# Kernel tuning notes

Measured on AMD Instinct MI355X. Metric: run time of the kernel, lower is better.

The kernel has to match this reference:

```python
import jax, jax.numpy as jnp
import numpy as np

HIND = 512
D = 256
P = 512          # 2*d Givens rotations
RHO_MAX = 9.0
DELTA = 1e-3
EPS = 1e-8
B = 32768


def setup_inputs() -> dict:
    key = jax.random.key(0)
    ks = jax.random.split(key, 12)
    f = lambda k, shape, sc=1.0: jax.random.normal(k, shape, dtype=jnp.float32) * sc
    return {
        "ent_embed": f(ks[0], (B, HIND)),
        "rel_embed": f(ks[1], (B, HIND)),
        "ent_label": f(ks[2], (B, HIND)),
        "sim": jax.random.uniform(ks[3], (B,), dtype=jnp.float32),
        # W_v: Linear(hind, d)
        "Wv": f(ks[4], (D, HIND), 0.05), "bv": jnp.zeros((D,), jnp.float32),
        # w_rho_ent: Linear(hind, 1), bias init 0.5
        "Wre": f(ks[5], (1, HIND), 0.05), "bre": jnp.full((1,), 0.5, jnp.float32),
        # w_rho_rel: Linear(hind, 1)
        "Wrr": f(ks[6], (1, HIND), 0.05), "brr": jnp.zeros((1,), jnp.float32),
        # W_theta: Linear(hind, P)
        "Wt": f(ks[7], (P, HIND), 0.05), "bt": jnp.zeros((P,), jnp.float32),
        "ga_rho": jnp.array([2.0], jnp.float32), "gb_rho": jnp.array([-0.5], jnp.float32),
        "ga_phi": jnp.array([2.0], jnp.float32), "gb_phi": jnp.array([-0.5], jnp.float32),
        # pre_mlp: Linear(hind,hind) -> ReLU -> Linear(hind,hind)
        "W1": f(ks[8], (HIND, HIND), 0.03), "b1": jnp.zeros((HIND,), jnp.float32),
        "W2": f(ks[9], (HIND, HIND), 0.03), "b2": jnp.zeros((HIND,), jnp.float32),
    }


def _l2norm(x):
    return x / (jnp.linalg.norm(x, axis=1, keepdims=True) + EPS)


def _forward(ent_embed, rel_embed, ent_label, sim,
             Wv, bv, Wre, bre, Wrr, brr, Wt, bt,
             ga_rho, gb_rho, ga_phi, gb_phi, W1, b1, W2, b2):
    pre = lambda x: x + jax.nn.relu(x @ W1.T + b1) @ W2.T + b2  # residual pre_mlp
    E_h, E_r, E_t = pre(ent_embed), pre(rel_embed), pre(ent_label)

    def to_polar(E):
        u = _l2norm(E @ Wv.T + bv)                       # [B, D] direction
        rho = jax.nn.softplus(E @ Wre.T + bre)           # [B, 1] radius
        return jnp.clip(rho, 0.0, RHO_MAX), u

    rho_h, u_h = to_polar(E_h)
    delta_rho = E_r @ Wrr.T + brr                        # [B, 1]
    thetas = jnp.pi * jnp.tanh(E_r @ Wt.T + bt)          # [B, P]

    simc = sim.reshape(-1, 1)
    g_rho = jax.nn.sigmoid(ga_rho * simc + gb_rho)
    g_phi = jax.nn.sigmoid(ga_phi * simc + gb_phi)
    rho_prime = jnp.clip(rho_h + delta_rho * g_rho, 0.0, RHO_MAX)

    # Sequential Givens rotations: pairs (m % D, (m % D + 1) % D)
    ii = jnp.arange(P, dtype=jnp.int32) % D
    jj = (ii + 1) % D
    c = jnp.cos(thetas).T                                # [P, B]
    s = jnp.sin(thetas).T

    def step(out, t):
        i, j, cm, sm = t
        ui, uj = out[:, i], out[:, j]
        out = out.at[:, i].set(cm * ui - sm * uj)
        out = out.at[:, j].set(sm * ui + cm * uj)
        return out, None

    u_rot, _ = jax.lax.scan(step, u_h, (ii, jj, c, s))
    u_rot = _l2norm(u_rot)

    # slerp(u_h -> u_rot, alpha = g_phi), lerp fallback when omega <= DELTA
    dot = jnp.clip(jnp.sum(u_h * u_rot, axis=1, keepdims=True), -1.0 + EPS, 1.0 - EPS)
    omega = jnp.arccos(dot)
    sin_omega = jnp.sin(omega)
    mask = (omega > DELTA).astype(u_h.dtype)
    s1 = jnp.sin((1.0 - g_phi) * omega) / (sin_omega + EPS)
    s2 = jnp.sin(g_phi * omega) / (sin_omega + EPS)
    u_prime = mask * (s1 * u_h + s2 * u_rot) + (1.0 - mask) * ((1.0 - g_phi) * u_h + g_phi * u_rot)
    u_prime = _l2norm(u_prime)

    rho_t, u_t = to_polar(E_t)
    # Lorentz lift: X = [cosh(rho), sinh(rho)*u]; inner = -x0*y0 + <xs, ys>
    Xh0, Xhs = jnp.cosh(rho_prime), jnp.sinh(rho_prime) * u_prime
    Xt0, Xts = jnp.cosh(rho_t), jnp.sinh(rho_t) * u_t
    score = (-Xh0 * Xt0 + jnp.sum(Xhs * Xts, axis=1, keepdims=True))[:, 0]  # [B]
    return score


def reference(ent_embed, rel_embed, ent_label, sim,
              Wv, bv, Wre, bre, Wrr, brr, Wt, bt,
              ga_rho, gb_rho, ga_phi, gb_phi, W1, b1, W2, b2):
    return _forward(ent_embed, rel_embed, ent_label, sim,
                    Wv, bv, Wre, bre, Wrr, brr, Wt, bt,
                    ga_rho, gb_rho, ga_phi, gb_phi, W1, b1, W2, b2)
```

## Files before the change

kernel.cpp:

```cpp
#include <hip/hip_runtime.h>
#include <cstdint>

#define NB 32768
#define HH 512

typedef __attribute__((ext_vector_type(8))) _Float16 f16x8;
typedef __attribute__((ext_vector_type(4))) float f32x4;
typedef __attribute__((ext_vector_type(4))) unsigned short us4v;

static __device__ __forceinline__ unsigned short f2h(float f) {
  _Float16 h = (_Float16)f;
  return __builtin_bit_cast(unsigned short, h);
}
static __device__ __forceinline__ float h2f(unsigned short u) {
  return (float)__builtin_bit_cast(_Float16, u);
}
static __device__ __forceinline__ void gl_lds16(const void* g, void* l) {
  __builtin_amdgcn_global_load_lds(
      (const __attribute__((address_space(1))) unsigned int*)g,
      (__attribute__((address_space(3))) unsigned int*)l, 16, 0, 0);
}
static __device__ __forceinline__ float wred(float v) {
#pragma unroll
  for (int off = 32; off > 0; off >>= 1) v += __shfl_xor(v, off);
  return v;
}
static __device__ __forceinline__ float sigm(float x) { return 1.f / (1.f + __expf(-x)); }
static __device__ __forceinline__ float tanh_fast(float x) {
  return 1.f - 2.f / (__expf(2.f * x) + 1.f);
}
static __device__ __forceinline__ float softplus_fast(float x) {
  return fmaxf(x, 0.f) + log1pf(__expf(-fabsf(x)));
}

__global__ __launch_bounds__(256) void prep_k(
    const float* __restrict__ W1, const float* __restrict__ Wv,
    const float* __restrict__ Wt, const float* __restrict__ Wre,
    const float* __restrict__ Wrr, const float* __restrict__ b2,
    const float* __restrict__ W2,
    unsigned short* __restrict__ W1h, unsigned short* __restrict__ Wvh,
    unsigned short* __restrict__ Wth, float* __restrict__ rho_raw,
    float* __restrict__ w2re, float* __restrict__ w2rr, float* __restrict__ rho_c) {
  __shared__ float red[4];
  const int bx = blockIdx.x, t = threadIdx.x;
  if (bx < 2560) {
    int i = bx * 256 + t;
    if (i < 98304) rho_raw[i] = 0.f;
    if (i < 262144) W1h[i] = f2h(W1[i]);
    else if (i < 393216) Wvh[i - 262144] = f2h(Wv[i - 262144]);
    else Wth[i - 393216] = f2h(Wt[i - 393216]);
  } else if (bx < 2562) {
    const float* ws = (bx == 2560) ? Wre : Wrr;
    float* wd = (bx == 2560) ? w2re : w2rr;
    float a0 = 0.f, a1 = 0.f;
    for (int j = 0; j < 512; ++j) {
      float wv = ws[j];
      a0 += wv * W2[j * 512 + t];
      a1 += wv * W2[j * 512 + t + 256];
    }
    wd[t] = a0;
    wd[t + 256] = a1;
  } else {
    const float* ws = (bx == 2562) ? Wre : Wrr;
    float p = b2[t] * ws[t] + b2[t + 256] * ws[t + 256];
    p = wred(p);
    if ((t & 63) == 0) red[t >> 6] = p;
    __syncthreads();
    if (t == 0) rho_c[bx - 2562] = red[0] + red[1] + red[2] + red[3];
  }
}

__global__ __launch_bounds__(256, 3) void gemm1_k(
    const float* __restrict__ x0, const float* __restrict__ x1,
    const float* __restrict__ x2, const unsigned short* __restrict__ W1h,
    const float* __restrict__ b1, const float* __restrict__ wre,
    const float* __restrict__ wrr, const float* __restrict__ w2re,
    const float* __restrict__ w2rr, unsigned short* __restrict__ Tbig,
    float* __restrict__ rho_raw) {
  __shared__ float Af[128 * 64];
  __shared__ unsigned short Bs[128 * 64];
  const int tid = threadIdx.x, lane = tid & 63, w = tid >> 6;
  const int by = blockIdx.y, ent = by >> 8;
  const long mloc = (long)(by & 255) * 128;
  const float* X = (ent == 0) ? x0 : (ent == 1) ? x1 : x2;
  const float* wsel = (ent < 2) ? wre : wrr;
  const float* w2sel = (ent < 2) ? w2re : w2rr;
  const int n0 = blockIdx.x * 128;
  const bool do_rx = (blockIdx.x == 0) && ((w & 1) == 0);
  const int wr = (w >> 1) * 64, wc = (w & 1) * 64;

  const int arow = w * 32 + (lane >> 4), acol = (lane & 15) * 4;
  const float* Ag = X + (mloc + arow) * HH + acol;
  float* Al = Af + arow * 64 + acol;
  const int brow = w * 32 + (lane >> 3), bcol = (lane & 7) * 8;
  const unsigned short* Bg = W1h + (long)(n0 + brow) * HH + bcol;
  unsigned short* Bl = Bs + brow * 64 + bcol;

  f32x4 acc[4][4] = {};
  float rx[4] = {0.f, 0.f, 0.f, 0.f};
  for (int kb = 0; kb < 8; ++kb) {
    const int ko = kb * 64;
#pragma unroll
    for (int q = 0; q < 8; ++q) gl_lds16(Ag + (long)(4 * q) * HH + ko, Al + (4 * q) * 64);
#pragma unroll
    for (int q = 0; q < 4; ++q) gl_lds16(Bg + (long)(8 * q) * HH + ko, Bl + (8 * q) * 64);
    __syncthreads();
#pragma unroll
    for (int ks = 0; ks < 2; ++ks) {
      const int kcol = ks * 32 + (lane >> 4) * 8;
      float wv[8];
      if (do_rx) {
        f32x4 wa = *(const f32x4*)(wsel + ko + kcol);
        f32x4 wb = *(const f32x4*)(wsel + ko + kcol + 4);
        wv[0] = wa[0]; wv[1] = wa[1]; wv[2] = wa[2]; wv[3] = wa[3];
        wv[4] = wb[0]; wv[5] = wb[1]; wv[6] = wb[2]; wv[7] = wb[3];
      }
      f16x8 af[4], bf[4];
#pragma unroll
      for (int i = 0; i < 4; ++i) {
        const float* ap = Af + (wr + i * 16 + (lane & 15)) * 64 + kcol;
        f32x4 a0 = *(const f32x4*)ap, a1 = *(const f32x4*)(ap + 4);
        f16x8 t;
        t[0] = (_Float16)a0[0]; t[1] = (_Float16)a0[1];
        t[2] = (_Float16)a0[2]; t[3] = (_Float16)a0[3];
        t[4] = (_Float16)a1[0]; t[5] = (_Float16)a1[1];
        t[6] = (_Float16)a1[2]; t[7] = (_Float16)a1[3];
        af[i] = t;
        if (do_rx) {
          rx[i] += a0[0] * wv[0] + a0[1] * wv[1] + a0[2] * wv[2] + a0[3] * wv[3] +
                   a1[0] * wv[4] + a1[1] * wv[5] + a1[2] * wv[6] + a1[3] * wv[7];
        }
        bf[i] = *(const f16x8*)(Bs + (wc + i * 16 + (lane & 15)) * 64 + kcol);
      }
#pragma unroll
      for (int i = 0; i < 4; ++i)
#pragma unroll
        for (int j = 0; j < 4; ++j)
          acc[i][j] = __builtin_amdgcn_mfma_f32_16x16x32_f16(af[i], bf[j], acc[i][j], 0, 0, 0);
    }
    __syncthreads();
  }

  const int cg = lane >> 4, cl = lane & 15;
  const long rbase = (long)ent * NB + mloc;
  float drow[4][4] = {};
#pragma unroll
  for (int mi = 0; mi < 4; ++mi) {
    const long row0 = rbase + wr + mi * 16 + cg * 4;
#pragma unroll
    for (int ni = 0; ni < 4; ++ni) {
      const int col = n0 + wc + ni * 16 + cl;
      const float bc = b1[col], w2v = w2sel[col];
#pragma unroll
      for (int r = 0; r < 4; ++r) {
        float v = fmaxf(acc[mi][ni][r] + bc, 0.f);
        Tbig[(row0 + r) * HH + col] = f2h(v);
        drow[mi][r] += v * w2v;
      }
    }
  }
#pragma unroll
  for (int mi = 0; mi < 4; ++mi)
#pragma unroll
    for (int r = 0; r < 4; ++r) {
      float s = drow[mi][r];
      s += __shfl_xor(s, 1); s += __shfl_xor(s, 2);
      s += __shfl_xor(s, 4); s += __shfl_xor(s, 8);
      if (cl == 0) atomicAdd(&rho_raw[rbase + wr + mi * 16 + cg * 4 + r], s);
    }
  if (do_rx) {
#pragma unroll
    for (int i = 0; i < 4; ++i) {
      float s = rx[i];
      s += __shfl_xor(s, 16); s += __shfl_xor(s, 32);
      if (lane < 16) atomicAdd(&rho_raw[rbase + wr + i * 16 + lane], s);
    }
  }
}

__global__ __launch_bounds__(256) void m2_k(
    const float* __restrict__ Wv, const float* __restrict__ Wt,
    const float* __restrict__ W2, const float* __restrict__ b2,
    const float* __restrict__ bv, const float* __restrict__ bt,
    unsigned short* __restrict__ M2v, unsigned short* __restrict__ M2t,
    float* __restrict__ bcv, float* __restrict__ bct) {
  __shared__ float rowL[512];
  __shared__ float red[4];
  const int b = blockIdx.x, t = threadIdx.x;
  int n; const float* src; unsigned short* dst; const float* badd; float* bdst;
  if (b < 256) { n = b; src = Wv + (long)n * 512; dst = M2v + (long)n * 512; badd = bv; bdst = bcv; }
  else { n = b - 256; src = Wt + (long)n * 512; dst = M2t + (long)n * 512; badd = bt; bdst = bct; }
  rowL[t] = src[t]; rowL[t + 256] = src[t + 256];
  __syncthreads();
  float a0 = 0.f, a1 = 0.f;
  for (int j = 0; j < 512; ++j) {
    float rv = rowL[j];
    a0 += rv * W2[(long)j * 512 + t];
    a1 += rv * W2[(long)j * 512 + t + 256];
  }
  dst[t] = f2h(a0);
  dst[t + 256] = f2h(a1);
  float p = b2[t] * rowL[t] + b2[t + 256] * rowL[t + 256];
  p = wred(p);
  if ((t & 63) == 0) red[t >> 6] = p;
  __syncthreads();
  if (t == 0) bdst[n] = badd[n] + red[0] + red[1] + red[2] + red[3];
}

__global__ __launch_bounds__(256, 3) void head_k(
    const float* __restrict__ x0, const float* __restrict__ x1,
    const float* __restrict__ x2, const unsigned short* __restrict__ Tbig,
    const unsigned short* __restrict__ Wvh, const unsigned short* __restrict__ Wth,
    const unsigned short* __restrict__ M2v, const unsigned short* __restrict__ M2t,
    const float* __restrict__ bcv, const float* __restrict__ bct,
    unsigned short* __restrict__ Uh, unsigned short* __restrict__ Ut,
    unsigned short* __restrict__ THh) {
  __shared__ float Af[128 * 64];
  __shared__ unsigned short Bs[128 * 64];
  unsigned short* As16 = (unsigned short*)Af;
  const int tid = threadIdx.x, lane = tid & 63, w = tid >> 6;
  const int bx = blockIdx.x;
  int ent, n0, ldo; long mloc;
  const float* X; const unsigned short *Wx, *Wm; const float* bias; unsigned short* Out;
  if (bx < 1024) {
    int nt = bx & 1, mt = bx >> 1;
    ent = mt >> 8; mloc = (long)(mt & 255) * 128; n0 = nt * 128; ldo = 256;
    X = ent ? x1 : x0; Wx = Wvh; Wm = M2v; bias = bcv; Out = ent ? Ut : Uh;
  } else {
    int t = bx - 1024, nt = t & 3, mt = t >> 2;
    ent = 2; mloc = (long)mt * 128; n0 = nt * 128; ldo = 512;
    X = x2; Wx = Wth; Wm = M2t; bias = bct; Out = THh;
  }
  const long trow = (long)ent * NB + mloc;
  const int wr = (w >> 1) * 64, wc = (w & 1) * 64;

  const int arow = w * 32 + (lane >> 4), acol = (lane & 15) * 4;
  const float* Ag = X + (mloc + arow) * HH + acol;
  float* Al = Af + arow * 64 + acol;
  const int srow = w * 32 + (lane >> 3), scol = (lane & 7) * 8;
  const unsigned short* Tg = Tbig + (trow + srow) * HH + scol;
  unsigned short* Sl = As16 + srow * 64 + scol;
  const int brow = srow, bcol = scol;
  unsigned short* Bl = Bs + brow * 64 + bcol;

  f32x4 acc[4][4] = {};
  for (int kb = 0; kb < 16; ++kb) {
    const int ko = (kb & 7) * 64;
    if (kb < 8) {
#pragma unroll
      for (int q = 0; q < 8; ++q) gl_lds16(Ag + (long)(4 * q) * HH + ko, Al + (4 * q) * 64);
    } else {
#pragma unroll
      for (int q = 0; q < 4; ++q) gl_lds16(Tg + (long)(8 * q) * HH + ko, Sl + (8 * q) * 64);
    }
    const unsigned short* Bg = ((kb < 8) ? Wx : Wm) + (long)(n0 + brow) * HH + bcol;
#pragma unroll
    for (int q = 0; q < 4; ++q) gl_lds16(Bg + (long)(8 * q) * HH + ko, Bl + (8 * q) * 64);
    __syncthreads();
#pragma unroll
    for (int ks = 0; ks < 2; ++ks) {
      const int kcol = ks * 32 + (lane >> 4) * 8;
      f16x8 af[4], bf[4];
#pragma unroll
      for (int i = 0; i < 4; ++i) {
        if (kb < 8) {
          const float* ap = Af + (wr + i * 16 + (lane & 15)) * 64 + kcol;
          f32x4 a0 = *(const f32x4*)ap, a1 = *(const f32x4*)(ap + 4);
          f16x8 t;
          t[0] = (_Float16)a0[0]; t[1] = (_Float16)a0[1];
          t[2] = (_Float16)a0[2]; t[3] = (_Float16)a0[3];
          t[4] = (_Float16)a1[0]; t[5] = (_Float16)a1[1];
          t[6] = (_Float16)a1[2]; t[7] = (_Float16)a1[3];
          af[i] = t;
        } else {
          af[i] = *(const f16x8*)(As16 + (wr + i * 16 + (lane & 15)) * 64 + kcol);
        }
        bf[i] = *(const f16x8*)(Bs + (wc + i * 16 + (lane & 15)) * 64 + kcol);
      }
#pragma unroll
      for (int i = 0; i < 4; ++i)
#pragma unroll
        for (int j = 0; j < 4; ++j)
          acc[i][j] = __builtin_amdgcn_mfma_f32_16x16x32_f16(af[i], bf[j], acc[i][j], 0, 0, 0);
    }
    __syncthreads();
  }

  const int cg = lane >> 4, cl = lane & 15;
#pragma unroll
  for (int mi = 0; mi < 4; ++mi) {
    const long row0 = mloc + wr + mi * 16 + cg * 4;
#pragma unroll
    for (int ni = 0; ni < 4; ++ni) {
      const int col = n0 + wc + ni * 16 + cl;
      const float bc = bias[col];
#pragma unroll
      for (int r = 0; r < 4; ++r)
        Out[(row0 + r) * (long)ldo + col] = f2h(acc[mi][ni][r] + bc);
    }
  }
}

__device__ __forceinline__ void givens_pass(float v[4], const float c[4],
                                            const float s[4], int lane) {
  float vn3 = __shfl_down(v[0], 1);
  float A = 1.f, Bc = 0.f;
#pragma unroll
  for (int k = 0; k < 4; ++k) {
    float vnext = (k < 3) ? v[k + 1] : vn3;
    bool skip = (lane == 63) && (k == 3);
    if (!skip) { Bc = s[k] * Bc + c[k] * vnext; A = s[k] * A; }
  }
  float iA = A, iB = Bc;
#pragma unroll
  for (int off = 1; off < 64; off <<= 1) {
    float pA = __shfl_up(iA, off);
    float pB = __shfl_up(iB, off);
    if (lane >= off) { iB = iA * pB + iB; iA = iA * pA; }
  }
  float eA = __shfl_up(iA, 1);
  float eB = __shfl_up(iB, 1);
  if (lane == 0) { eA = 1.f; eB = 0.f; }
  float v0g = __shfl(v[0], 0);
  float K = eA * v0g + eB;
  float out[4];
#pragma unroll
  for (int k = 0; k < 4; ++k) {
    float vnext = (k < 3) ? v[k + 1] : vn3;
    bool skip = (lane == 63) && (k == 3);
    if (!skip) {
      out[k] = c[k] * K - s[k] * vnext;
      K = s[k] * K + c[k] * vnext;
    } else out[k] = 0.f;
  }
  float K255 = __shfl(K, 63);
  float c255 = __shfl(c[3], 63);
  float s255 = __shfl(s[3], 63);
  float o0 = __shfl(out[0], 0);
  if (lane == 63) out[3] = c255 * K255 - s255 * o0;
  if (lane == 0) out[0] = s255 * K255 + c255 * o0;
  v[0] = out[0]; v[1] = out[1]; v[2] = out[2]; v[3] = out[3];
}

__global__ __launch_bounds__(256) void final_k(
    const unsigned short* __restrict__ Uh, const unsigned short* __restrict__ Ut,
    const unsigned short* __restrict__ THh, const float* __restrict__ rho_raw,
    const float* __restrict__ rho_c, const float* __restrict__ sim,
    const float* __restrict__ bre, const float* __restrict__ brr,
    const float* __restrict__ ga_rho, const float* __restrict__ gb_rho,
    const float* __restrict__ ga_phi, const float* __restrict__ gb_phi,
    float* __restrict__ out) {
  const int lane = threadIdx.x & 63;
  const int b = blockIdx.x * 4 + (threadIdx.x >> 6);

  us4v h4 = *(const us4v*)(Uh + (long)b * 256 + lane * 4);
  us4v t4 = *(const us4v*)(Ut + (long)b * 256 + lane * 4);
  us4v a4 = *(const us4v*)(THh + (long)b * 512 + lane * 4);
  us4v b4 = *(const us4v*)(THh + (long)b * 512 + 256 + lane * 4);

  const float PI_F = 3.14159265358979f;
  float vh[4], vt[4], cA[4], sA[4], cB[4], sB[4];
#pragma unroll
  for (int k = 0; k < 4; ++k) {
    vh[k] = h2f(h4[k]); vt[k] = h2f(t4[k]);
    float aa = PI_F * tanh_fast(h2f(a4[k]));
    sA[k] = __sinf(aa); cA[k] = __cosf(aa);
    float ab = PI_F * tanh_fast(h2f(b4[k]));
    sB[k] = __sinf(ab); cB[k] = __cosf(ab);
  }

  float ssq = wred(vh[0] * vh[0] + vh[1] * vh[1] + vh[2] * vh[2] + vh[3] * vh[3]);
  float invh = 1.f / (sqrtf(ssq) + 1e-8f);
  float u[4], v[4];
#pragma unroll
  for (int k = 0; k < 4; ++k) { u[k] = vh[k] * invh; v[k] = u[k]; }

  givens_pass(v, cA, sA, lane);
  givens_pass(v, cB, sB, lane);

  float ssr = wred(v[0] * v[0] + v[1] * v[1] + v[2] * v[2] + v[3] * v[3]);
  float invr = 1.f / (sqrtf(ssr) + 1e-8f);
  float ur[4];
#pragma unroll
  for (int k = 0; k < 4; ++k) ur[k] = v[k] * invr;

  float dt = wred(u[0] * ur[0] + u[1] * ur[1] + u[2] * ur[2] + u[3] * ur[3]);
  dt = fminf(fmaxf(dt, -1.f + 1e-8f), 1.f - 1e-8f);
  float omega = acosf(dt);
  float sino = sqrtf(fmaxf(1.f - dt * dt, 0.f));
  float sb = sim[b];
  float gphi = sigm(ga_phi[0] * sb + gb_phi[0]);
  float s1, s2;
  if (omega > 0.001f) {
    s1 = __sinf((1.f - gphi) * omega) / (sino + 1e-8f);
    s2 = __sinf(gphi * omega) / (sino + 1e-8f);
  } else {
    s1 = 1.f - gphi;
    s2 = gphi;
  }
  float up[4];
#pragma unroll
  for (int k = 0; k < 4; ++k) up[k] = s1 * u[k] + s2 * ur[k];
  float ssp = wred(up[0] * up[0] + up[1] * up[1] + up[2] * up[2] + up[3] * up[3]);
  float invp = 1.f / (sqrtf(ssp) + 1e-8f);
  float sst = wred(vt[0] * vt[0] + vt[1] * vt[1] + vt[2] * vt[2] + vt[3] * vt[3]);
  float invt = 1.f / (sqrtf(sst) + 1e-8f);
  float dp = wred(up[0] * vt[0] + up[1] * vt[1] + up[2] * vt[2] + up[3] * vt[3]) * invp * invt;

  float rh = fminf(fmaxf(softplus_fast(rho_raw[b] + rho_c[0] + bre[0]), 0.f), 9.f);
  float rt = fminf(fmaxf(softplus_fast(rho_raw[NB + b] + rho_c[0] + bre[0]), 0.f), 9.f);
  float dR = rho_raw[2 * NB + b] + rho_c[1] + brr[0];
  float grho = sigm(ga_rho[0] * sb + gb_rho[0]);
  float rp = fminf(fmaxf(rh + dR * grho, 0.f), 9.f);
  float er = __expf(rp), eri = __expf(-rp);
  float et = __expf(rt), eti = __expf(-rt);
  float score = -0.25f * (er + eri) * (et + eti) + 0.25f * (er - eri) * (et - eti) * dp;
  if (lane == 0) out[b] = score;
}

extern "C" void kernel_launch(void* const* d_in, const int* in_sizes, int n_in,
                              void* d_out, int out_size, void* d_ws, size_t ws_size,
                              hipStream_t stream) {
  (void)in_sizes; (void)n_in;
  const float* x0 = (const float*)d_in[0];
  const float* x2 = (const float*)d_in[1];
  const float* x1 = (const float*)d_in[2];
  const float* sim = (const float*)d_in[3];
  const float* Wv = (const float*)d_in[4];
  const float* bv = (const float*)d_in[5];
  const float* Wre = (const float*)d_in[6];
  const float* bre = (const float*)d_in[7];
  const float* Wrr = (const float*)d_in[8];
  const float* brr = (const float*)d_in[9];
  const float* Wt = (const float*)d_in[10];
  const float* bt = (const float*)d_in[11];
  const float* ga_rho = (const float*)d_in[12];
  const float* gb_rho = (const float*)d_in[13];
  const float* ga_phi = (const float*)d_in[14];
  const float* gb_phi = (const float*)d_in[15];
  const float* W1 = (const float*)d_in[16];
  const float* b1 = (const float*)d_in[17];
  const float* W2 = (const float*)d_in[18];
  const float* b2 = (const float*)d_in[19];

  const size_t NEEDED = 169745416ULL;
  if (ws_size < NEEDED) {
    (void)hipMemsetAsync(d_out, 0, (size_t)out_size * sizeof(float), stream);
    return;
  }
  char* ws = (char*)d_ws;
  unsigned short* Tbig = (unsigned short*)ws;
  unsigned short* Uh = (unsigned short*)(ws + 100663296);
  unsigned short* Ut = (unsigned short*)(ws + 117440512);
  unsigned short* THh = (unsigned short*)(ws + 134217728);
  float* rho_raw = (float*)(ws + 167772160);
  unsigned short* W1h = (unsigned short*)(ws + 168165376);
  unsigned short* Wvh = (unsigned short*)(ws + 168689664);
  unsigned short* Wth = (unsigned short*)(ws + 168951808);
  unsigned short* M2v = (unsigned short*)(ws + 169476096);
  unsigned short* M2t = W1h;
  float* w2re = (float*)(ws + 169738240);
  float* w2rr = (float*)(ws + 169740288);
  float* bcv = (float*)(ws + 169742336);
  float* bct = (float*)(ws + 169743360);
  float* rho_c = (float*)(ws + 169745408);

  prep_k<<<dim3(2564), dim3(256), 0, stream>>>(
      W1, Wv, Wt, Wre, Wrr, b2, W2, W1h, Wvh, Wth, rho_raw, w2re, w2rr, rho_c);

  gemm1_k<<<dim3(4, 768), dim3(256), 0, stream>>>(
      x0, x1, x2, W1h, b1, Wre, Wrr, w2re, w2rr, Tbig, rho_raw);

  m2_k<<<dim3(768), dim3(256), 0, stream>>>(Wv, Wt, W2, b2, bv, bt, M2v, M2t, bcv, bct);

  head_k<<<dim3(2048), dim3(256), 0, stream>>>(
      x0, x1, x2, Tbig, Wvh, Wth, M2v, M2t, bcv, bct, Uh, Ut, THh);

  final_k<<<dim3(8192), dim3(256), 0, stream>>>(
      Uh, Ut, THh, rho_raw, rho_c, sim, bre, brr, ga_rho, gb_rho, ga_phi, gb_phi,
      (float*)d_out);
}
```

Baseline: 594.0 us.

## Fuse first MLP GEMM with projection heads, keeping hidden activations in LDS

Merges gemm1_k and head_k into one kernel that processes 32-row tiles. Each tile converts X to fp16 into swizzled LDS, computes relu(X W1^T + b1) into LDS, and then runs the Wv/M2v or Wt/M2t projections from LDS. This drops the 100MB fp16 hidden tensor round trip through global memory and the rho_raw zeroing and global atomics. In exchange, B fragments are read straight from global/L2 with no LDS staging, the row tiles are small (32 rows), and the whole K loop sits in one block, which may limit MFMA efficiency and occupancy.

New measurement: 749.3 us. +26.2%, slower.

```diff
diff --git a/kernel.cpp b/kernel.cpp
--- a/kernel.cpp
+++ b/kernel.cpp
@@ -14,11 +14,6 @@
 }
 static __device__ __forceinline__ float h2f(unsigned short u) {
   return (float)__builtin_bit_cast(_Float16, u);
-}
-static __device__ __forceinline__ void gl_lds16(const void* g, void* l) {
-  __builtin_amdgcn_global_load_lds(
-      (const __attribute__((address_space(1))) unsigned int*)g,
-      (__attribute__((address_space(3))) unsigned int*)l, 16, 0, 0);
 }
 static __device__ __forceinline__ float wred(float v) {
 #pragma unroll
@@ -39,13 +34,12 @@
     const float* __restrict__ Wrr, const float* __restrict__ b2,
     const float* __restrict__ W2,
     unsigned short* __restrict__ W1h, unsigned short* __restrict__ Wvh,
-    unsigned short* __restrict__ Wth, float* __restrict__ rho_raw,
+    unsigned short* __restrict__ Wth,
     float* __restrict__ w2re, float* __restrict__ w2rr, float* __restrict__ rho_c) {
   __shared__ float red[4];
   const int bx = blockIdx.x, t = threadIdx.x;
   if (bx < 2560) {
     int i = bx * 256 + t;
-    if (i < 98304) rho_raw[i] = 0.f;
     if (i < 262144) W1h[i] = f2h(W1[i]);
     else if (i < 393216) Wvh[i - 262144] = f2h(Wv[i - 262144]);
     else Wth[i - 393216] = f2h(Wt[i - 393216]);
@@ -70,114 +64,6 @@
   }
 }
 
-__global__ __launch_bounds__(256, 3) void gemm1_k(
-    const float* __restrict__ x0, const float* __restrict__ x1,
-    const float* __restrict__ x2, const unsigned short* __restrict__ W1h,
-    const float* __restrict__ b1, const float* __restrict__ wre,
-    const float* __restrict__ wrr, const float* __restrict__ w2re,
-    const float* __restrict__ w2rr, unsigned short* __restrict__ Tbig,
-    float* __restrict__ rho_raw) {
-  __shared__ float Af[128 * 64];
-  __shared__ unsigned short Bs[128 * 64];
-  const int tid = threadIdx.x, lane = tid & 63, w = tid >> 6;
-  const int by = blockIdx.y, ent = by >> 8;
-  const long mloc = (long)(by & 255) * 128;
-  const float* X = (ent == 0) ? x0 : (ent == 1) ? x1 : x2;
-  const float* wsel = (ent < 2) ? wre : wrr;
-  const float* w2sel = (ent < 2) ? w2re : w2rr;
-  const int n0 = blockIdx.x * 128;
-  const bool do_rx = (blockIdx.x == 0) && ((w & 1) == 0);
-  const int wr = (w >> 1) * 64, wc = (w & 1) * 64;
-
-  const int arow = w * 32 + (lane >> 4), acol = (lane & 15) * 4;
-  const float* Ag = X + (mloc + arow) * HH + acol;
-  float* Al = Af + arow * 64 + acol;
-  const int brow = w * 32 + (lane >> 3), bcol = (lane & 7) * 8;
-  const unsigned short* Bg = W1h + (long)(n0 + brow) * HH + bcol;
-  unsigned short* Bl = Bs + brow * 64 + bcol;
-
-  f32x4 acc[4][4] = {};
-  float rx[4] = {0.f, 0.f, 0.f, 0.f};
-  for (int kb = 0; kb < 8; ++kb) {
-    const int ko = kb * 64;
-#pragma unroll
-    for (int q = 0; q < 8; ++q) gl_lds16(Ag + (long)(4 * q) * HH + ko, Al + (4 * q) * 64);
-#pragma unroll
-    for (int q = 0; q < 4; ++q) gl_lds16(Bg + (long)(8 * q) * HH + ko, Bl + (8 * q) * 64);
-    __syncthreads();
-#pragma unroll
-    for (int ks = 0; ks < 2; ++ks) {
-      const int kcol = ks * 32 + (lane >> 4) * 8;
-      float wv[8];
-      if (do_rx) {
-        f32x4 wa = *(const f32x4*)(wsel + ko + kcol);
-        f32x4 wb = *(const f32x4*)(wsel + ko + kcol + 4);
-        wv[0] = wa[0]; wv[1] = wa[1]; wv[2] = wa[2]; wv[3] = wa[3];
-        wv[4] = wb[0]; wv[5] = wb[1]; wv[6] = wb[2]; wv[7] = wb[3];
-      }
-      f16x8 af[4], bf[4];
-#pragma unroll
-      for (int i = 0; i < 4; ++i) {
-        const float* ap = Af + (wr + i * 16 + (lane & 15)) * 64 + kcol;
-        f32x4 a0 = *(const f32x4*)ap, a1 = *(const f32x4*)(ap + 4);
-        f16x8 t;
-        t[0] = (_Float16)a0[0]; t[1] = (_Float16)a0[1];
-        t[2] = (_Float16)a0[2]; t[3] = (_Float16)a0[3];
-        t[4] = (_Float16)a1[0]; t[5] = (_Float16)a1[1];
-        t[6] = (_Float16)a1[2]; t[7] = (_Float16)a1[3];
-        af[i] = t;
-        if (do_rx) {
-          rx[i] += a0[0] * wv[0] + a0[1] * wv[1] + a0[2] * wv[2] + a0[3] * wv[3] +
-                   a1[0] * wv[4] + a1[1] * wv[5] + a1[2] * wv[6] + a1[3] * wv[7];
-        }
-        bf[i] = *(const f16x8*)(Bs + (wc + i * 16 + (lane & 15)) * 64 + kcol);
-      }
-#pragma unroll
-      for (int i = 0; i < 4; ++i)
-#pragma unroll
-        for (int j = 0; j < 4; ++j)
-          acc[i][j] = __builtin_amdgcn_mfma_f32_16x16x32_f16(af[i], bf[j], acc[i][j], 0, 0, 0);
-    }
-    __syncthreads();
-  }
-
-  const int cg = lane >> 4, cl = lane & 15;
-  const long rbase = (long)ent * NB + mloc;
-  float drow[4][4] = {};
-#pragma unroll
-  for (int mi = 0; mi < 4; ++mi) {
-    const long row0 = rbase + wr + mi * 16 + cg * 4;
-#pragma unroll
-    for (int ni = 0; ni < 4; ++ni) {
-      const int col = n0 + wc + ni * 16 + cl;
-      const float bc = b1[col], w2v = w2sel[col];
-#pragma unroll
-      for (int r = 0; r < 4; ++r) {
-        float v = fmaxf(acc[mi][ni][r] + bc, 0.f);
-        Tbig[(row0 + r) * HH + col] = f2h(v);
-        drow[mi][r] += v * w2v;
-      }
-    }
-  }
-#pragma unroll
-  for (int mi = 0; mi < 4; ++mi)
-#pragma unroll
-    for (int r = 0; r < 4; ++r) {
-      float s = drow[mi][r];
-      s += __shfl_xor(s, 1); s += __shfl_xor(s, 2);
-      s += __shfl_xor(s, 4); s += __shfl_xor(s, 8);
-      if (cl == 0) atomicAdd(&rho_raw[rbase + wr + mi * 16 + cg * 4 + r], s);
-    }
-  if (do_rx) {
-#pragma unroll
-    for (int i = 0; i < 4; ++i) {
-      float s = rx[i];
-      s += __shfl_xor(s, 16); s += __shfl_xor(s, 32);
-      if (lane < 16) atomicAdd(&rho_raw[rbase + wr + i * 16 + lane], s);
-    }
-  }
-}
-
 __global__ __launch_bounds__(256) void m2_k(
     const float* __restrict__ Wv, const float* __restrict__ Wt,
     const float* __restrict__ W2, const float* __restrict__ b2,
@@ -207,97 +93,144 @@
   if (t == 0) bdst[n] = badd[n] + red[0] + red[1] + red[2] + red[3];
 }
 
-__global__ __launch_bounds__(256, 3) void head_k(
+template <int NF>
+static __device__ __forceinline__ void gemm_half(
+    const unsigned short* As,
+    const unsigned short* __restrict__ Bg,
+    int nw, int cg, int cl, f32x4 (&acc)[2][NF]) {
+#pragma unroll 2
+  for (int kb = 0; kb < 16; ++kb) {
+    const int kcol = kb * 32 + cg * 8;
+    f16x8 af[2];
+#pragma unroll
+    for (int i = 0; i < 2; ++i) {
+      const int row = i * 16 + cl;
+      const int bo = (row * 1024 + kcol * 2) ^ ((row & 7) << 4);
+      af[i] = *(const f16x8*)((const char*)As + bo);
+    }
+#pragma unroll
+    for (int j = 0; j < NF; ++j) {
+      const f16x8 bj = *(const f16x8*)(Bg + (long)(nw + j * 16 + cl) * HH + kcol);
+#pragma unroll
+      for (int i = 0; i < 2; ++i)
+        acc[i][j] = __builtin_amdgcn_mfma_f32_16x16x32_f16(af[i], bj, acc[i][j], 0, 0, 0);
+    }
+  }
+}
+
+__global__ __launch_bounds__(256, 2) void fused_k(
     const float* __restrict__ x0, const float* __restrict__ x1,
-    const float* __restrict__ x2, const unsigned short* __restrict__ Tbig,
-    const unsigned short* __restrict__ Wvh, const unsigned short* __restrict__ Wth,
-    const unsigned short* __restrict__ M2v, const unsigned short* __restrict__ M2t,
-    const float* __restrict__ bcv, const float* __restrict__ bct,
-    unsigned short* __restrict__ Uh, unsigned short* __restrict__ Ut,
-    unsigned short* __restrict__ THh) {
-  __shared__ float Af[128 * 64];
-  __shared__ unsigned short Bs[128 * 64];
-  unsigned short* As16 = (unsigned short*)Af;
+    const float* __restrict__ x2, const unsigned short* __restrict__ W1h,
+    const float* __restrict__ b1, const float* __restrict__ wre,
+    const float* __restrict__ wrr, const float* __restrict__ w2re,
+    const float* __restrict__ w2rr, const unsigned short* __restrict__ Wvh,
+    const unsigned short* __restrict__ Wth, const unsigned short* __restrict__ M2v,
+    const unsigned short* __restrict__ M2t, const float* __restrict__ bcv,
+    const float* __restrict__ bct, unsigned short* __restrict__ Uh,
+    unsigned short* __restrict__ Ut, unsigned short* __restrict__ THh,
+    float* __restrict__ rho_raw) {
+  __shared__ unsigned short Xh[32 * 512];
+  __shared__ unsigned short Ts[32 * 512];
+  __shared__ float rxp[32];
+  __shared__ float rtp[32];
   const int tid = threadIdx.x, lane = tid & 63, w = tid >> 6;
+  const int cg = lane >> 4, cl = lane & 15;
   const int bx = blockIdx.x;
-  int ent, n0, ldo; long mloc;
-  const float* X; const unsigned short *Wx, *Wm; const float* bias; unsigned short* Out;
-  if (bx < 1024) {
-    int nt = bx & 1, mt = bx >> 1;
-    ent = mt >> 8; mloc = (long)(mt & 255) * 128; n0 = nt * 128; ldo = 256;
-    X = ent ? x1 : x0; Wx = Wvh; Wm = M2v; bias = bcv; Out = ent ? Ut : Uh;
+  const int ent = bx >> 10;
+  const long mloc = (long)(bx & 1023) * 32;
+  const float* X = (ent == 0) ? x0 : (ent == 1) ? x1 : x2;
+  const float* wsel = (ent < 2) ? wre : wrr;
+  const float* w2sel = (ent < 2) ? w2re : w2rr;
+
+  if (tid < 32) rtp[tid] = 0.f;
+
+  {
+    const int col = lane * 8;
+    const f32x4 wv0 = *(const f32x4*)(wsel + col);
+    const f32x4 wv1 = *(const f32x4*)(wsel + col + 4);
+#pragma unroll
+    for (int q = 0; q < 8; ++q) {
+      const int row = q * 4 + w;
+      const float* gp = X + (mloc + row) * HH + col;
+      const f32x4 a0 = *(const f32x4*)gp;
+      const f32x4 a1 = *(const f32x4*)(gp + 4);
+      f16x8 hx;
+      hx[0] = (_Float16)a0[0]; hx[1] = (_Float16)a0[1];
+      hx[2] = (_Float16)a0[2]; hx[3] = (_Float16)a0[3];
+      hx[4] = (_Float16)a1[0]; hx[5] = (_Float16)a1[1];
+      hx[6] = (_Float16)a1[2]; hx[7] = (_Float16)a1[3];
+      const int bo = (row * 1024 + col * 2) ^ ((row & 7) << 4);
+      *(f16x8*)((char*)Xh + bo) = hx;
+      float p = a0[0] * wv0[0] + a0[1] * wv0[1] + a0[2] * wv0[2] + a0[3] * wv0[3] +
+                a1[0] * wv1[0] + a1[1] * wv1[1] + a1[2] * wv1[2] + a1[3] * wv1[3];
+      p = wred(p);
+      if (lane == 0) rxp[row] = p;
+    }
+  }
+  __syncthreads();
+
+  {
+    f32x4 acc[2][8] = {};
+    gemm_half<8>(Xh, W1h, w * 128, cg, cl, acc);
+    float drow[2][4] = {{0.f, 0.f, 0.f, 0.f}, {0.f, 0.f, 0.f, 0.f}};
+#pragma unroll
+    for (int i = 0; i < 2; ++i)
+#pragma unroll
+      for (int j = 0; j < 8; ++j) {
+        const int col = w * 128 + j * 16 + cl;
+        const float bc = b1[col], w2v = w2sel[col];
+#pragma unroll
+        for (int r = 0; r < 4; ++r) {
+          const int row = i * 16 + cg * 4 + r;
+          const float v = fmaxf(acc[i][j][r] + bc, 0.f);
+          const int bo = (row * 1024 + col * 2) ^ ((row & 7) << 4);
+          *(unsigned short*)((char*)Ts + bo) = f2h(v);
+          drow[i][r] += v * w2v;
+        }
+      }
+#pragma unroll
+    for (int i = 0; i < 2; ++i)
+#pragma unroll
+      for (int r = 0; r < 4; ++r) {
+        float s = drow[i][r];
+        s += __shfl_xor(s, 1); s += __shfl_xor(s, 2);
+        s += __shfl_xor(s, 4); s += __shfl_xor(s, 8);
+        if (cl == 0) atomicAdd(&rtp[i * 16 + cg * 4 + r], s);
+      }
+  }
+  __syncthreads();
+
+  if (tid < 32) rho_raw[(long)ent * NB + mloc + tid] = rxp[tid] + rtp[tid];
+
+  if (ent < 2) {
+    unsigned short* Out = ent ? Ut : Uh;
+    f32x4 acc[2][4] = {};
+    gemm_half<4>(Xh, Wvh, w * 64, cg, cl, acc);
+    gemm_half<4>(Ts, M2v, w * 64, cg, cl, acc);
+#pragma unroll
+    for (int i = 0; i < 2; ++i)
+#pragma unroll
+      for (int j = 0; j < 4; ++j) {
+        const int col = w * 64 + j * 16 + cl;
+        const float bc = bcv[col];
+#pragma unroll
+        for (int r = 0; r < 4; ++r)
+          Out[(mloc + i * 16 + cg * 4 + r) * 256 + col] = f2h(acc[i][j][r] + bc);
+      }
   } else {
-    int t = bx - 1024, nt = t & 3, mt = t >> 2;
-    ent = 2; mloc = (long)mt * 128; n0 = nt * 128; ldo = 512;
-    X = x2; Wx = Wth; Wm = M2t; bias = bct; Out = THh;
-  }
-  const long trow = (long)ent * NB + mloc;
-  const int wr = (w >> 1) * 64, wc = (w & 1) * 64;
-
-  const int arow = w * 32 + (lane >> 4), acol = (lane & 15) * 4;
-  const float* Ag = X + (mloc + arow) * HH + acol;
-  float* Al = Af + arow * 64 + acol;
-  const int srow = w * 32 + (lane >> 3), scol = (lane & 7) * 8;
-  const unsigned short* Tg = Tbig + (trow + srow) * HH + scol;
-  unsigned short* Sl = As16 + srow * 64 + scol;
-  const int brow = srow, bcol = scol;
-  unsigned short* Bl = Bs + brow * 64 + bcol;
-
-  f32x4 acc[4][4] = {};
-  for (int kb = 0; kb < 16; ++kb) {
-    const int ko = (kb & 7) * 64;
-    if (kb < 8) {
-#pragma unroll
-      for (int q = 0; q < 8; ++q) gl_lds16(Ag + (long)(4 * q) * HH + ko, Al + (4 * q) * 64);
-    } else {
-#pragma unroll
-      for (int q = 0; q < 4; ++q) gl_lds16(Tg + (long)(8 * q) * HH + ko, Sl + (8 * q) * 64);
-    }
-    const unsigned short* Bg = ((kb < 8) ? Wx : Wm) + (long)(n0 + brow) * HH + bcol;
-#pragma unroll
-    for (int q = 0; q < 4; ++q) gl_lds16(Bg + (long)(8 * q) * HH + ko, Bl + (8 * q) * 64);
-    __syncthreads();
-#pragma unroll
-    for (int ks = 0; ks < 2; ++ks) {
-      const int kcol = ks * 32 + (lane >> 4) * 8;
-      f16x8 af[4], bf[4];
-#pragma unroll
-      for (int i = 0; i < 4; ++i) {
-        if (kb < 8) {
-          const float* ap = Af + (wr + i * 16 + (lane & 15)) * 64 + kcol;
-          f32x4 a0 = *(const f32x4*)ap, a1 = *(const f32x4*)(ap + 4);
-          f16x8 t;
-          t[0] = (_Float16)a0[0]; t[1] = (_Float16)a0[1];
-          t[2] = (_Float16)a0[2]; t[3] = (_Float16)a0[3];
-          t[4] = (_Float16)a1[0]; t[5] = (_Float16)a1[1];
-          t[6] = (_Float16)a1[2]; t[7] = (_Float16)a1[3];
-          af[i] = t;
-        } else {
-          af[i] = *(const f16x8*)(As16 + (wr + i * 16 + (lane & 15)) * 64 + kcol);
-        }
-        bf[i] = *(const f16x8*)(Bs + (wc + i * 16 + (lane & 15)) * 64 + kcol);
+    f32x4 acc[2][8] = {};
+    gemm_half<8>(Xh, Wth, w * 128, cg, cl, acc);
+    gemm_half<8>(Ts, M2t, w * 128, cg, cl, acc);
+#pragma unroll
+    for (int i = 0; i < 2; ++i)
+#pragma unroll
+      for (int j = 0; j < 8; ++j) {
+        const int col = w * 128 + j * 16 + cl;
+        const float bc = bct[col];
+#pragma unroll
+        for (int r = 0; r < 4; ++r)
+          THh[(mloc + i * 16 + cg * 4 + r) * (long)HH + col] = f2h(acc[i][j][r] + bc);
       }
-#pragma unroll
-      for (int i = 0; i < 4; ++i)
-#pragma unroll
-        for (int j = 0; j < 4; ++j)
-          acc[i][j] = __builtin_amdgcn_mfma_f32_16x16x32_f16(af[i], bf[j], acc[i][j], 0, 0, 0);
-    }
-    __syncthreads();
-  }
-
-  const int cg = lane >> 4, cl = lane & 15;
-#pragma unroll
-  for (int mi = 0; mi < 4; ++mi) {
-    const long row0 = mloc + wr + mi * 16 + cg * 4;
-#pragma unroll
-    for (int ni = 0; ni < 4; ++ni) {
-      const int col = n0 + wc + ni * 16 + cl;
-      const float bc = bias[col];
-#pragma unroll
-      for (int r = 0; r < 4; ++r)
-        Out[(row0 + r) * (long)ldo + col] = f2h(acc[mi][ni][r] + bc);
-    }
   }
 }
 
@@ -443,38 +376,35 @@
   const float* W2 = (const float*)d_in[18];
   const float* b2 = (const float*)d_in[19];
 
-  const size_t NEEDED = 169745416ULL;
+  const size_t NEEDED = 69606408ULL;
   if (ws_size < NEEDED) {
     (void)hipMemsetAsync(d_out, 0, (size_t)out_size * sizeof(float), stream);
     return;
   }
   char* ws = (char*)d_ws;
-  unsigned short* Tbig = (unsigned short*)ws;
-  unsigned short* Uh = (unsigned short*)(ws + 100663296);
-  unsigned short* Ut = (unsigned short*)(ws + 117440512);
-  unsigned short* THh = (unsigned short*)(ws + 134217728);
-  float* rho_raw = (float*)(ws + 167772160);
-  unsigned short* W1h = (unsigned short*)(ws + 168165376);
-  unsigned short* Wvh = (unsigned short*)(ws + 168689664);
-  unsigned short* Wth = (unsigned short*)(ws + 168951808);
-  unsigned short* M2v = (unsigned short*)(ws + 169476096);
-  unsigned short* M2t = W1h;
-  float* w2re = (float*)(ws + 169738240);
-  float* w2rr = (float*)(ws + 169740288);
-  float* bcv = (float*)(ws + 169742336);
-  float* bct = (float*)(ws + 169743360);
-  float* rho_c = (float*)(ws + 169745408);
+  unsigned short* Uh = (unsigned short*)ws;
+  unsigned short* Ut = (unsigned short*)(ws + 16777216);
+  unsigned short* THh = (unsigned short*)(ws + 33554432);
+  float* rho_raw = (float*)(ws + 67108864);
+  unsigned short* W1h = (unsigned short*)(ws + 67502080);
+  unsigned short* Wvh = (unsigned short*)(ws + 68026368);
+  unsigned short* Wth = (unsigned short*)(ws + 68288512);
+  unsigned short* M2v = (unsigned short*)(ws + 68812800);
+  unsigned short* M2t = (unsigned short*)(ws + 69074944);
+  float* w2re = (float*)(ws + 69599232);
+  float* w2rr = (float*)(ws + 69601280);
+  float* bcv = (float*)(ws + 69603328);
+  float* bct = (float*)(ws + 69604352);
+  float* rho_c = (float*)(ws + 69606400);
 
   prep_k<<<dim3(2564), dim3(256), 0, stream>>>(
-      W1, Wv, Wt, Wre, Wrr, b2, W2, W1h, Wvh, Wth, rho_raw, w2re, w2rr, rho_c);
-
-  gemm1_k<<<dim3(4, 768), dim3(256), 0, stream>>>(
-      x0, x1, x2, W1h, b1, Wre, Wrr, w2re, w2rr, Tbig, rho_raw);
+      W1, Wv, Wt, Wre, Wrr, b2, W2, W1h, Wvh, Wth, w2re, w2rr, rho_c);
 
   m2_k<<<dim3(768), dim3(256), 0, stream>>>(Wv, Wt, W2, b2, bv, bt, M2v, M2t, bcv, bct);
 
-  head_k<<<dim3(2048), dim3(256), 0, stream>>>(
-      x0, x1, x2, Tbig, Wvh, Wth, M2v, M2t, bcv, bct, Uh, Ut, THh);
+  fused_k<<<dim3(3072), dim3(256), 0, stream>>>(
+      x0, x1, x2, W1h, b1, Wre, Wrr, w2re, w2rr, Wvh, Wth, M2v, M2t, bcv, bct,
+      Uh, Ut, THh, rho_raw);
 
   final_k<<<dim3(8192), dim3(256), 0, stream>>>(
       Uh, Ut, THh, rho_raw, rho_c, sim, bre, brr, ga_rho, gb_rho, ga_phi, gb_phi,
```
